# Optimization experiments

Hardware: AMD Instinct MI355X
Metric: run time of the kernel (lower is better)

## Reference

```python
import jax, jax.numpy as jnp
import numpy as np


def setup_inputs() -> dict:
    key = jax.random.key(0)
    kq, kc = jax.random.split(key)
    query = jax.random.normal(kq, (64, 768), dtype=jnp.float32)
    corpus = jax.random.normal(kc, (500000, 768), dtype=jnp.float32)
    return {"query": query, "corpus": corpus, "k": 16}


def reference(query, corpus, k):
    # cosine similarity: (q @ c.T) / (|q|[:,None] * |c|[None,:])  -> [B, N]
    sim = jnp.einsum("bd,nd->bn", query, corpus)
    qn = jnp.linalg.norm(query, axis=1)   # [B]
    cn = jnp.linalg.norm(corpus, axis=1)  # [N]
    sim = sim / (qn[:, None] * cn[None, :])
    # top-k most similar corpus entries per query (largest=True)
    values, indices = jax.lax.top_k(sim, k)  # [B, k], [B, k]
    return values, indices
```

## Files before the change

kernel.cpp:

```cpp
#include <hip/hip_runtime.h>
#include <hip/hip_bf16.h>

#define D 768
#define NQ 64
#define NT 128
#define KC 64
#define NCH (D / KC)
#define TPB 256
#define SIMSTRIDE 133
#define NS 8

typedef float    f32x4 __attribute__((ext_vector_type(4)));
typedef _Float16 h16x8 __attribute__((ext_vector_type(8)));

typedef const void __attribute__((address_space(1)))* gas_ptr;
typedef void __attribute__((address_space(3)))* las_ptr;

__device__ __forceinline__ bool kbetter(float v1, int i1, float v2, int i2) {
    return (v1 > v2) || (v1 == v2 && i1 < i2);
}

__device__ __forceinline__ void topk_insert(float (&tv)[16], int (&ti)[16], float v, int idx) {
    if (!kbetter(v, idx, tv[15], ti[15])) return;
    tv[15] = v; ti[15] = idx;
    #pragma unroll
    for (int s = 15; s >= 1; --s) {
        bool sw = kbetter(tv[s], ti[s], tv[s-1], ti[s-1]);
        float av = sw ? tv[s] : tv[s-1];
        float bv = sw ? tv[s-1] : tv[s];
        int   ai = sw ? ti[s] : ti[s-1];
        int   bi = sw ? ti[s-1] : ti[s];
        tv[s-1] = av; tv[s] = bv; ti[s-1] = ai; ti[s] = bi;
    }
}

__device__ __forceinline__ void bitonic16(float (&v)[16], int (&ix)[16]) {
    #pragma unroll
    for (int d = 8; d >= 1; d >>= 1) {
        #pragma unroll
        for (int i = 0; i < 16; ++i) {
            if ((i & d) == 0) {
                int j = i | d;
                bool sw = kbetter(v[j], ix[j], v[i], ix[i]);
                float av = sw ? v[j] : v[i];
                float bv = sw ? v[i] : v[j];
                int   ai = sw ? ix[j] : ix[i];
                int   bi = sw ? ix[i] : ix[j];
                v[i] = av; v[j] = bv; ix[i] = ai; ix[j] = bi;
            }
        }
    }
}

__device__ __forceinline__ void lane_merge(float (&v)[16], int (&ix)[16], int mask) {
    float pv[16]; int pix[16];
    #pragma unroll
    for (int i = 0; i < 16; ++i) {
        pv[i]  = __shfl_xor(v[15 - i], mask);
        pix[i] = __shfl_xor(ix[15 - i], mask);
    }
    #pragma unroll
    for (int i = 0; i < 16; ++i) {
        if (kbetter(pv[i], pix[i], v[i], ix[i])) { v[i] = pv[i]; ix[i] = pix[i]; }
    }
    bitonic16(v, ix);
}

__device__ __forceinline__ void sort64(float& v, int& ix, int l) {
    #pragma unroll
    for (int k = 2; k <= 64; k <<= 1) {
        #pragma unroll
        for (int j = k >> 1; j >= 1; j >>= 1) {
            float ov = __shfl_xor(v, j);
            int   oi = __shfl_xor(ix, j);
            bool dirDesc = ((l & k) == 0);
            bool lower   = ((l & j) == 0);
            bool takeBetter = (lower == dirDesc);
            bool ob = kbetter(ov, oi, v, ix);
            if (takeBetter == ob) { v = ov; ix = oi; }
        }
    }
}

__global__ __launch_bounds__(256)
void prep_kernel(const float* __restrict__ query, _Float16* __restrict__ qfh,
                 _Float16* __restrict__ qfl) {
    int b = blockIdx.x, t = threadIdx.x;
    const float* row = query + b * D;
    float vals[3]; float s = 0.f;
    #pragma unroll
    for (int j = 0; j < 3; ++j) { vals[j] = row[t + 256 * j]; s += vals[j] * vals[j]; }
    #pragma unroll
    for (int m = 1; m < 64; m <<= 1) s += __shfl_xor(s, m);
    __shared__ float ws4[4];
    if ((t & 63) == 0) ws4[t >> 6] = s;
    __syncthreads();
    float qn = sqrtf(ws4[0] + ws4[1] + ws4[2] + ws4[3]);
    int qf = b >> 4;
    #pragma unroll
    for (int j = 0; j < 3; ++j) {
        int col = t + 256 * j;
        float vn = vals[j] / qn;
        _Float16 h = (_Float16)vn;
        float r = vn - (float)h;
        _Float16 l2 = (_Float16)(r * 2048.0f);
        int cc = col >> 6, kk = (col >> 5) & 1, unit = (col >> 3) & 3, sub = col & 7;
        int lane = (b & 15) + unit * 16;
        size_t off = ((((size_t)cc * 2 + kk) * 4 + qf) * 64 + lane) * 8 + sub;
        qfh[off] = h;
        qfl[off] = l2;
    }
}

__global__ __launch_bounds__(TPB, 2)
void sim_topk_kernel(const float* __restrict__ corpus,
                     const _Float16* __restrict__ qfh,
                     const _Float16* __restrict__ qfl,
                     float2* __restrict__ cand,
                     int N, int NB) {
    __shared__ __align__(16) float lds[2 * NT * KC];
    int t = threadIdx.x, w = t >> 6, l = t & 63;
    int b = blockIdx.x;
    long n0 = (long)b * NT;

    f32x4 accH[4][2], accX[4][2];
    #pragma unroll
    for (int qf = 0; qf < 4; ++qf)
        #pragma unroll
        for (int nfl = 0; nfl < 2; ++nfl) { accH[qf][nfl] = (f32x4)(0.f); accX[qf][nfl] = (f32x4)(0.f); }
    float psum[2] = {0.f, 0.f};

    auto STAGE = [&](int c, int buf) {
        #pragma unroll
        for (int j = 0; j < 8; ++j) {
            int U = t + TPB * j;
            int row = U >> 4, unit = U & 15;
            long grow = n0 + row; if (grow >= N) grow = N - 1;
            int su = unit ^ (row & 15);
            const float* src = corpus + (size_t)grow * D + c * KC + su * 4;
            float* dst = &lds[buf * (NT * KC) + (size_t)U * 4];
            __builtin_amdgcn_global_load_lds((gas_ptr)(const void*)src, (las_ptr)(void*)dst, 16, 0, 0);
        }
    };

    STAGE(0, 0);
    __syncthreads();

    for (int c = 0; c < NCH; ++c) {
        int buf = c & 1;
        if (c + 1 < NCH) STAGE(c + 1, buf ^ 1);

        const float* bufp = &lds[buf * (NT * KC)];
        #pragma unroll
        for (int kk = 0; kk < 2; ++kk) {
            h16x8 qh[4], ql[4];
            #pragma unroll
            for (int qf = 0; qf < 4; ++qf) {
                size_t qoff = ((((size_t)c * 2 + kk) * 4 + qf) * 64 + l) * 8;
                qh[qf] = *(const h16x8*)(qfh + qoff);
                ql[qf] = *(const h16x8*)(qfl + qoff);
            }
            #pragma unroll
            for (int nfl = 0; nfl < 2; ++nfl) {
                int row = w * 32 + nfl * 16 + (l & 15);
                int u0 = kk * 8 + ((l >> 4) << 1);
                f32x4 x0 = *(const f32x4*)(bufp + row * KC + ((u0 ^ (row & 15)) << 2));
                f32x4 x1 = *(const f32x4*)(bufp + row * KC + (((u0 + 1) ^ (row & 15)) << 2));
                h16x8 hi, lo;
                float ps = 0.f;
                #pragma unroll
                for (int i2 = 0; i2 < 4; ++i2) {
                    float v0 = x0[i2]; _Float16 h0 = (_Float16)v0;
                    hi[i2] = h0; lo[i2] = (_Float16)((v0 - (float)h0) * 2048.0f);
                    ps += v0 * v0;
                    float v1 = x1[i2]; _Float16 h1 = (_Float16)v1;
                    hi[4 + i2] = h1; lo[4 + i2] = (_Float16)((v1 - (float)h1) * 2048.0f);
                    ps += v1 * v1;
                }
                psum[nfl] += ps;
                #pragma unroll
                for (int qf = 0; qf < 4; ++qf) {
                    accH[qf][nfl] = __builtin_amdgcn_mfma_f32_16x16x32_f16(qh[qf], hi, accH[qf][nfl], 0, 0, 0);
                    accX[qf][nfl] = __builtin_amdgcn_mfma_f32_16x16x32_f16(qh[qf], lo, accX[qf][nfl], 0, 0, 0);
                    accX[qf][nfl] = __builtin_amdgcn_mfma_f32_16x16x32_f16(ql[qf], hi, accX[qf][nfl], 0, 0, 0);
                }
            }
        }
        __syncthreads();
    }

    float cnv[2];
    #pragma unroll
    for (int nfl = 0; nfl < 2; ++nfl) {
        float s = psum[nfl];
        s += __shfl_xor(s, 16);
        s += __shfl_xor(s, 32);
        cnv[nfl] = sqrtf(s);
    }

    float* sim = (float*)lds;
    #pragma unroll
    for (int nfl = 0; nfl < 2; ++nfl) {
        int n = w * 32 + nfl * 16 + (l & 15);
        #pragma unroll
        for (int qf = 0; qf < 4; ++qf) {
            #pragma unroll
            for (int r = 0; r < 4; ++r) {
                int q = qf * 16 + ((l >> 4) << 2) + r;
                float dot = accH[qf][nfl][r] + accX[qf][nfl][r] * (1.0f / 2048.0f);
                sim[q * SIMSTRIDE + n] = dot / cnv[nfl];
            }
        }
    }
    __syncthreads();

    int q = t >> 2, cc = t & 3;
    float tv[16]; int ti[16];
    #pragma unroll
    for (int s = 0; s < 16; ++s) { tv[s] = -INFINITY; ti[s] = 0x7fffffff; }
    for (int i = 0; i < 32; ++i) {
        int n = cc * 32 + i;
        long g = n0 + n;
        if (g < N) topk_insert(tv, ti, sim[q * SIMSTRIDE + n], (int)g);
    }
    lane_merge(tv, ti, 1);
    lane_merge(tv, ti, 2);
    if ((l & 3) == 0) {
        float2* dst = cand + ((size_t)q * NB + b) * 16;
        #pragma unroll
        for (int s = 0; s < 16; ++s) dst[s] = make_float2(tv[s], __int_as_float(ti[s]));
    }
}

__global__ __launch_bounds__(256)
void merge1_kernel(const float2* __restrict__ cand, float2* __restrict__ cand2, int NB) {
    int q = blockIdx.x >> 3, seg = blockIdx.x & (NS - 1);
    int t = threadIdx.x, w = t >> 6, l = t & 63;
    int total = NB * 16;
    int chunk = (total + NS - 1) / NS;
    int e0 = seg * chunk, e1 = min(total, e0 + chunk);
    const float2* src = cand + (size_t)q * total;
    float tv[16]; int ti[16];
    #pragma unroll
    for (int s = 0; s < 16; ++s) { tv[s] = -INFINITY; ti[s] = 0x7fffffff; }
    for (int e = e0 + t; e < e1; e += 256) {
        float2 ce = src[e];
        topk_insert(tv, ti, ce.x, __float_as_int(ce.y));
    }
    lane_merge(tv, ti, 1);  lane_merge(tv, ti, 2);  lane_merge(tv, ti, 4);
    lane_merge(tv, ti, 8);  lane_merge(tv, ti, 16); lane_merge(tv, ti, 32);
    __shared__ float2 stage[64];
    if (l == 0) {
        #pragma unroll
        for (int s = 0; s < 16; ++s) stage[w * 16 + s] = make_float2(tv[s], __int_as_float(ti[s]));
    }
    __syncthreads();
    if (t < 64) {
        float2 ce = stage[t];
        float v = ce.x; int ix = __float_as_int(ce.y);
        sort64(v, ix, t);
        if (t < 16) cand2[((size_t)q * NS + seg) * 16 + t] = make_float2(v, __int_as_float(ix));
    }
}

__global__ __launch_bounds__(64)
void merge2_kernel(const float2* __restrict__ cand2, float* __restrict__ out) {
    int q = blockIdx.x, l = threadIdx.x;
    const float2* src = cand2 + (size_t)q * (NS * 16);
    float2 a = src[l], b = src[l + 64];
    float v1 = a.x; int i1 = __float_as_int(a.y);
    float v2 = b.x; int i2 = __float_as_int(b.y);
    sort64(v1, i1, l);
    sort64(v2, i2, l);
    float sv = __shfl(v2, (l - 16) & 63);
    int   si = __shfl(i2, (l - 16) & 63);
    float mv = (l < 16) ? v1 : ((l < 32) ? sv : -INFINITY);
    int   mi = (l < 16) ? i1 : ((l < 32) ? si : 0x7fffffff);
    sort64(mv, mi, l);
    if (l < 16) {
        out[q * 16 + l]           = mv;
        out[NQ * 16 + q * 16 + l] = (float)mi;
    }
}

extern "C" void kernel_launch(void* const* d_in, const int* in_sizes, int n_in,
                              void* d_out, int out_size, void* d_ws, size_t ws_size,
                              hipStream_t stream) {
    const float* query  = (const float*)d_in[0];
    const float* corpus = (const float*)d_in[1];
    int N  = in_sizes[1] / D;
    int NB = (N + NT - 1) / NT;
    char* ws = (char*)d_ws;
    _Float16* qfh = (_Float16*)ws;
    _Float16* qfl = (_Float16*)(ws + 98304);
    float2*  cand = (float2*)(ws + 196608);
    size_t candBytes = (size_t)NQ * NB * 16 * sizeof(float2);
    float2* cand2 = (float2*)(ws + 196608 + candBytes);
    float*   out  = (float*)d_out;

    prep_kernel<<<NQ, 256, 0, stream>>>(query, qfh, qfl);
    sim_topk_kernel<<<NB, TPB, 0, stream>>>(corpus, qfh, qfl, cand, N, NB);
    merge1_kernel<<<NQ * NS, 256, 0, stream>>>(cand, cand2, NB);
    merge2_kernel<<<NQ, 64, 0, stream>>>(cand2, out);
}
```

Before: 512.3 us.

## Make similarity kernel persistent with 4-deep LDS pipeline and manual waitcnt scheduling

The sim_topk kernel becomes persistent: a fixed grid of 256 blocks of 512 threads walks contiguous ranges of 64-row corpus tiles. Each tile is split into six 128-wide K chunks, staged through a 4-buffer ring in dynamic LDS with direct global-to-LDS loads. Query fragments are double-buffered in registers, and explicit vmcnt waits plus raw barriers keep loads in flight across tile boundaries. The aim is to hide HBM latency and launch/tail overhead. The cost is twice as many per-tile candidates for the merge stage, plus fragile hand-tuned wait counts.

```diff
diff --git a/kernel.cpp b/kernel.cpp
--- a/kernel.cpp
+++ b/kernel.cpp
@@ -3,12 +3,19 @@
 
 #define D 768
 #define NQ 64
-#define NT 128
-#define KC 64
-#define NCH (D / KC)
-#define TPB 256
-#define SIMSTRIDE 133
+#define NT 64
+#define KC 128
+#define NCHT 6
+#define TPB 512
+#define NBUF 4
+#define SIMST 65
 #define NS 8
+#define GRID 256
+
+#define LDS_BUF_F   (NT * KC)
+#define LDS_SIM_F   (NBUF * LDS_BUF_F)
+#define LDS_CN_F    (LDS_SIM_F + NQ * SIMST)
+#define LDS_BYTES   ((LDS_CN_F + NT) * 4)
 
 typedef float    f32x4 __attribute__((ext_vector_type(4)));
 typedef _Float16 h16x8 __attribute__((ext_vector_type(8)));
@@ -104,139 +111,173 @@
         _Float16 h = (_Float16)vn;
         float r = vn - (float)h;
         _Float16 l2 = (_Float16)(r * 2048.0f);
-        int cc = col >> 6, kk = (col >> 5) & 1, unit = (col >> 3) & 3, sub = col & 7;
+        int cm = col >> 7, ks = (col >> 5) & 3, unit = (col >> 3) & 3, sub = col & 7;
         int lane = (b & 15) + unit * 16;
-        size_t off = ((((size_t)cc * 2 + kk) * 4 + qf) * 64 + lane) * 8 + sub;
+        size_t off = ((((size_t)cm * 4 + ks) * 4 + qf) * 64 + lane) * 8 + sub;
         qfh[off] = h;
         qfl[off] = l2;
     }
 }
+
+struct QF { h16x8 h[2][4]; h16x8 l[2][4]; };
 
 __global__ __launch_bounds__(TPB, 2)
 void sim_topk_kernel(const float* __restrict__ corpus,
                      const _Float16* __restrict__ qfh,
                      const _Float16* __restrict__ qfl,
                      float2* __restrict__ cand,
-                     int N, int NB) {
-    __shared__ __align__(16) float lds[2 * NT * KC];
+                     int N, int NTILES) {
+    extern __shared__ __align__(16) float lds[];
+    float* simF = lds + LDS_SIM_F;
+    float* cnF  = lds + LDS_CN_F;
+
     int t = threadIdx.x, w = t >> 6, l = t & 63;
+    int qfp = w >> 2, nfl = w & 3;
     int b = blockIdx.x;
-    long n0 = (long)b * NT;
-
-    f32x4 accH[4][2], accX[4][2];
-    #pragma unroll
-    for (int qf = 0; qf < 4; ++qf)
-        #pragma unroll
-        for (int nfl = 0; nfl < 2; ++nfl) { accH[qf][nfl] = (f32x4)(0.f); accX[qf][nfl] = (f32x4)(0.f); }
-    float psum[2] = {0.f, 0.f};
-
-    auto STAGE = [&](int c, int buf) {
-        #pragma unroll
-        for (int j = 0; j < 8; ++j) {
-            int U = t + TPB * j;
-            int row = U >> 4, unit = U & 15;
-            long grow = n0 + row; if (grow >= N) grow = N - 1;
-            int su = unit ^ (row & 15);
-            const float* src = corpus + (size_t)grow * D + c * KC + su * 4;
-            float* dst = &lds[buf * (NT * KC) + (size_t)U * 4];
+    int q0 = NTILES / GRID, R = NTILES % GRID;
+    int tstart = b * q0 + min(b, R);
+    int cnt = q0 + (b < R ? 1 : 0);
+    int NC = cnt * NCHT;
+
+    f32x4 accH[2], accX[2];
+    #pragma unroll
+    for (int j = 0; j < 2; ++j) { accH[j] = (f32x4)(0.f); accX[j] = (f32x4)(0.f); }
+    float psum = 0.f;
+
+    QF qA, qB;
+
+    auto QLOAD = [&](int cmq, QF& qd) {
+        #pragma unroll
+        for (int ks = 0; ks < 4; ++ks)
+            #pragma unroll
+            for (int j = 0; j < 2; ++j) {
+                size_t off = ((((size_t)cmq * 4 + ks) * 4 + (qfp * 2 + j)) * 64 + l) * 8;
+                qd.h[j][ks] = *(const h16x8*)(qfh + off);
+                qd.l[j][ks] = *(const h16x8*)(qfl + off);
+            }
+    };
+
+    auto STAGE = [&](int k) {
+        int tile = tstart + k / NCHT;
+        int cm = k % NCHT;
+        float* dbase = lds + (k & 3) * LDS_BUF_F;
+        #pragma unroll
+        for (int jj = 0; jj < 4; ++jj) {
+            int U = t + TPB * jj;
+            int row = U >> 5, g = U & 31;
+            int grow = tile * NT + row;
+            if (grow > N - 1) grow = N - 1;
+            int gs = g ^ (row & 7);
+            const float* src = corpus + (size_t)grow * D + cm * KC + gs * 4;
+            float* dst = dbase + (size_t)U * 4;
             __builtin_amdgcn_global_load_lds((gas_ptr)(const void*)src, (las_ptr)(void*)dst, 16, 0, 0);
         }
     };
 
-    STAGE(0, 0);
-    __syncthreads();
-
-    for (int c = 0; c < NCH; ++c) {
-        int buf = c & 1;
-        if (c + 1 < NCH) STAGE(c + 1, buf ^ 1);
-
-        const float* bufp = &lds[buf * (NT * KC)];
-        #pragma unroll
-        for (int kk = 0; kk < 2; ++kk) {
-            h16x8 qh[4], ql[4];
-            #pragma unroll
-            for (int qf = 0; qf < 4; ++qf) {
-                size_t qoff = ((((size_t)c * 2 + kk) * 4 + qf) * 64 + l) * 8;
-                qh[qf] = *(const h16x8*)(qfh + qoff);
-                ql[qf] = *(const h16x8*)(qfl + qoff);
-            }
-            #pragma unroll
-            for (int nfl = 0; nfl < 2; ++nfl) {
-                int row = w * 32 + nfl * 16 + (l & 15);
-                int u0 = kk * 8 + ((l >> 4) << 1);
-                f32x4 x0 = *(const f32x4*)(bufp + row * KC + ((u0 ^ (row & 15)) << 2));
-                f32x4 x1 = *(const f32x4*)(bufp + row * KC + (((u0 + 1) ^ (row & 15)) << 2));
-                h16x8 hi, lo;
-                float ps = 0.f;
-                #pragma unroll
-                for (int i2 = 0; i2 < 4; ++i2) {
-                    float v0 = x0[i2]; _Float16 h0 = (_Float16)v0;
-                    hi[i2] = h0; lo[i2] = (_Float16)((v0 - (float)h0) * 2048.0f);
-                    ps += v0 * v0;
-                    float v1 = x1[i2]; _Float16 h1 = (_Float16)v1;
-                    hi[4 + i2] = h1; lo[4 + i2] = (_Float16)((v1 - (float)h1) * 2048.0f);
-                    ps += v1 * v1;
-                }
-                psum[nfl] += ps;
-                #pragma unroll
-                for (int qf = 0; qf < 4; ++qf) {
-                    accH[qf][nfl] = __builtin_amdgcn_mfma_f32_16x16x32_f16(qh[qf], hi, accH[qf][nfl], 0, 0, 0);
-                    accX[qf][nfl] = __builtin_amdgcn_mfma_f32_16x16x32_f16(qh[qf], lo, accX[qf][nfl], 0, 0, 0);
-                    accX[qf][nfl] = __builtin_amdgcn_mfma_f32_16x16x32_f16(ql[qf], hi, accX[qf][nfl], 0, 0, 0);
-                }
-            }
-        }
-        __syncthreads();
-    }
-
-    float cnv[2];
-    #pragma unroll
-    for (int nfl = 0; nfl < 2; ++nfl) {
-        float s = psum[nfl];
+    auto COMPUTE = [&](int bidx, QF& qc) {
+        const float* bp = lds + bidx * LDS_BUF_F;
+        int rw = nfl * 16 + (l & 15);
+        int cg = l >> 4;
+        #pragma unroll
+        for (int ks = 0; ks < 4; ++ks) {
+            int g0 = ks * 8 + cg * 2;
+            f32x4 x0 = *(const f32x4*)(bp + rw * KC + ((g0 ^ (rw & 7)) << 2));
+            f32x4 x1 = *(const f32x4*)(bp + rw * KC + (((g0 + 1) ^ (rw & 7)) << 2));
+            h16x8 hi, lo;
+            float ps = 0.f;
+            #pragma unroll
+            for (int i2 = 0; i2 < 4; ++i2) {
+                float v0 = x0[i2]; _Float16 h0 = (_Float16)v0;
+                hi[i2] = h0; lo[i2] = (_Float16)((v0 - (float)h0) * 2048.0f);
+                ps += v0 * v0;
+                float v1 = x1[i2]; _Float16 h1 = (_Float16)v1;
+                hi[4 + i2] = h1; lo[4 + i2] = (_Float16)((v1 - (float)h1) * 2048.0f);
+                ps += v1 * v1;
+            }
+            if (qfp == 0) psum += ps;
+            #pragma unroll
+            for (int j = 0; j < 2; ++j) {
+                accH[j] = __builtin_amdgcn_mfma_f32_16x16x32_f16(qc.h[j][ks], hi, accH[j], 0, 0, 0);
+                accX[j] = __builtin_amdgcn_mfma_f32_16x16x32_f16(qc.h[j][ks], lo, accX[j], 0, 0, 0);
+                accX[j] = __builtin_amdgcn_mfma_f32_16x16x32_f16(qc.l[j][ks], hi, accX[j], 0, 0, 0);
+            }
+        }
+    };
+
+    auto TAIL = [&](int tile) {
+        float s = psum;
         s += __shfl_xor(s, 16);
         s += __shfl_xor(s, 32);
-        cnv[nfl] = sqrtf(s);
-    }
-
-    float* sim = (float*)lds;
-    #pragma unroll
-    for (int nfl = 0; nfl < 2; ++nfl) {
-        int n = w * 32 + nfl * 16 + (l & 15);
-        #pragma unroll
-        for (int qf = 0; qf < 4; ++qf) {
+        if (qfp == 0 && l < 16) cnF[nfl * 16 + l] = sqrtf(s);
+        asm volatile("s_waitcnt lgkmcnt(0)" ::: "memory");
+        __builtin_amdgcn_s_barrier();
+        int n = nfl * 16 + (l & 15);
+        float inv = 1.0f / cnF[n];
+        #pragma unroll
+        for (int j = 0; j < 2; ++j)
             #pragma unroll
             for (int r = 0; r < 4; ++r) {
-                int q = qf * 16 + ((l >> 4) << 2) + r;
-                float dot = accH[qf][nfl][r] + accX[qf][nfl][r] * (1.0f / 2048.0f);
-                sim[q * SIMSTRIDE + n] = dot / cnv[nfl];
-            }
-        }
-    }
-    __syncthreads();
-
-    int q = t >> 2, cc = t & 3;
-    float tv[16]; int ti[16];
-    #pragma unroll
-    for (int s = 0; s < 16; ++s) { tv[s] = -INFINITY; ti[s] = 0x7fffffff; }
-    for (int i = 0; i < 32; ++i) {
-        int n = cc * 32 + i;
-        long g = n0 + n;
-        if (g < N) topk_insert(tv, ti, sim[q * SIMSTRIDE + n], (int)g);
-    }
-    lane_merge(tv, ti, 1);
-    lane_merge(tv, ti, 2);
-    if ((l & 3) == 0) {
-        float2* dst = cand + ((size_t)q * NB + b) * 16;
-        #pragma unroll
-        for (int s = 0; s < 16; ++s) dst[s] = make_float2(tv[s], __int_as_float(ti[s]));
+                int q = qfp * 32 + j * 16 + (l >> 4) * 4 + r;
+                float dot = accH[j][r] + accX[j][r] * (1.0f / 2048.0f);
+                simF[q * SIMST + n] = dot * inv;
+            }
+        asm volatile("s_waitcnt lgkmcnt(0)" ::: "memory");
+        __builtin_amdgcn_s_barrier();
+        int q = t >> 3, sl = t & 7;
+        float tv[16]; int ti[16];
+        #pragma unroll
+        for (int s2 = 0; s2 < 16; ++s2) { tv[s2] = -INFINITY; ti[s2] = 0x7fffffff; }
+        #pragma unroll
+        for (int i = 0; i < 8; ++i) {
+            int n2 = sl * 8 + i;
+            int g = tile * NT + n2;
+            if (g < N) topk_insert(tv, ti, simF[q * SIMST + n2], g);
+        }
+        lane_merge(tv, ti, 1); lane_merge(tv, ti, 2); lane_merge(tv, ti, 4);
+        if (sl == 0) {
+            float2* dst = cand + ((size_t)q * NTILES + tile) * 16;
+            #pragma unroll
+            for (int s2 = 0; s2 < 16; ++s2) dst[s2] = make_float2(tv[s2], __int_as_float(ti[s2]));
+        }
+        #pragma unroll
+        for (int j = 0; j < 2; ++j) { accH[j] = (f32x4)(0.f); accX[j] = (f32x4)(0.f); }
+        psum = 0.f;
+    };
+
+    auto BODY = [&](int cc, QF& qc, QF& qn) {
+        int cm = cc % NCHT;
+        if (cc + 1 < NC) QLOAD((cc + 1) % NCHT, qn);
+        if (cc + 2 < NC) STAGE(cc + 2);
+        if (cc == 0) {
+            asm volatile("s_waitcnt vmcnt(20)" ::: "memory");
+        } else if (cc + 2 >= NC) {
+            if (cc + 1 < NC) { asm volatile("s_waitcnt vmcnt(20)" ::: "memory"); }
+            else             { asm volatile("s_waitcnt vmcnt(0)"  ::: "memory"); }
+        } else if (cm == 0) {
+            asm volatile("s_waitcnt vmcnt(40)" ::: "memory");
+        } else {
+            asm volatile("s_waitcnt vmcnt(24)" ::: "memory");
+        }
+        __builtin_amdgcn_sched_barrier(0);
+        __builtin_amdgcn_s_barrier();
+        __builtin_amdgcn_sched_barrier(0);
+        COMPUTE(cc & 3, qc);
+        if (cm == NCHT - 1) TAIL(tstart + cc / NCHT);
+    };
+
+    STAGE(0); STAGE(1); QLOAD(0, qA);
+    int half = NC >> 1;
+    for (int m = 0; m < half; ++m) {
+        BODY(2 * m,     qA, qB);
+        BODY(2 * m + 1, qB, qA);
     }
 }
 
 __global__ __launch_bounds__(256)
-void merge1_kernel(const float2* __restrict__ cand, float2* __restrict__ cand2, int NB) {
+void merge1_kernel(const float2* __restrict__ cand, float2* __restrict__ cand2, int NTILES) {
     int q = blockIdx.x >> 3, seg = blockIdx.x & (NS - 1);
     int t = threadIdx.x, w = t >> 6, l = t & 63;
-    int total = NB * 16;
+    int total = NTILES * 16;
     int chunk = (total + NS - 1) / NS;
     int e0 = seg * chunk, e1 = min(total, e0 + chunk);
     const float2* src = cand + (size_t)q * total;
@@ -288,18 +329,21 @@
                               hipStream_t stream) {
     const float* query  = (const float*)d_in[0];
     const float* corpus = (const float*)d_in[1];
-    int N  = in_sizes[1] / D;
-    int NB = (N + NT - 1) / NT;
+    int N      = in_sizes[1] / D;
+    int NTILES = (N + NT - 1) / NT;
     char* ws = (char*)d_ws;
     _Float16* qfh = (_Float16*)ws;
     _Float16* qfl = (_Float16*)(ws + 98304);
     float2*  cand = (float2*)(ws + 196608);
-    size_t candBytes = (size_t)NQ * NB * 16 * sizeof(float2);
+    size_t candBytes = (size_t)NQ * NTILES * 16 * sizeof(float2);
     float2* cand2 = (float2*)(ws + 196608 + candBytes);
     float*   out  = (float*)d_out;
 
+    (void)hipFuncSetAttribute((const void*)sim_topk_kernel,
+                              hipFuncAttributeMaxDynamicSharedMemorySize, LDS_BYTES);
+
     prep_kernel<<<NQ, 256, 0, stream>>>(query, qfh, qfl);
-    sim_topk_kernel<<<NB, TPB, 0, stream>>>(corpus, qfh, qfl, cand, N, NB);
-    merge1_kernel<<<NQ * NS, 256, 0, stream>>>(cand, cand2, NB);
+    sim_topk_kernel<<<GRID, TPB, LDS_BYTES, stream>>>(corpus, qfh, qfl, cand, N, NTILES);
+    merge1_kernel<<<NQ * NS, 256, 0, stream>>>(cand, cand2, NTILES);
     merge2_kernel<<<NQ, 64, 0, stream>>>(cand2, out);
 }
```

Result: slower. 752.6 us (+46.9%).

## Convert corpus to fp16 hi/lo once at staging and use 512-thread blocks

Applied to the files above, without the earlier changes.

Corpus tiles are no longer copied straight into LDS as fp32 with global_load_lds. Each chunk is now loaded into registers, split into fp16 hi/lo halves once, and written to padded LDS buffers, while the next chunk's global loads overlap the MFMA work on the current one. Block size doubles to 512 threads with one 16-row fragment per wave, corpus norms go through LDS, and top-k uses 8 lanes per query. The aim is to stop each wave redoing the fp32-to-fp16 split and to raise occupancy, at the cost of more VGPR pressure from register staging and an extra LDS round trip.

```diff
diff --git a/kernel.cpp b/kernel.cpp
--- a/kernel.cpp
+++ b/kernel.cpp
@@ -5,16 +5,20 @@
 #define NQ 64
 #define NT 128
 #define KC 64
-#define NCH (D / KC)
-#define TPB 256
-#define SIMSTRIDE 133
+#define NCHT 12
+#define TPB 512
+#define SIMST 133
 #define NS 8
+
+#define HST 72
+#define BUF_HALVES (NT * HST)
+#define BUF_STRIDE (2 * BUF_HALVES)
+#define LDS_CN_BYTE (2 * BUF_STRIDE * 2)
+#define LDS_BYTES (LDS_CN_BYTE + NT * 4)
 
 typedef float    f32x4 __attribute__((ext_vector_type(4)));
 typedef _Float16 h16x8 __attribute__((ext_vector_type(8)));
-
-typedef const void __attribute__((address_space(1)))* gas_ptr;
-typedef void __attribute__((address_space(3)))* las_ptr;
+typedef _Float16 h16x4 __attribute__((ext_vector_type(4)));
 
 __device__ __forceinline__ bool kbetter(float v1, int i1, float v2, int i2) {
     return (v1 > v2) || (v1 == v2 && i1 < i2);
@@ -112,131 +116,138 @@
     }
 }
 
-__global__ __launch_bounds__(TPB, 2)
+__global__ __launch_bounds__(TPB, 4)
 void sim_topk_kernel(const float* __restrict__ corpus,
                      const _Float16* __restrict__ qfh,
                      const _Float16* __restrict__ qfl,
                      float2* __restrict__ cand,
-                     int N, int NB) {
-    __shared__ __align__(16) float lds[2 * NT * KC];
+                     int N, int NTILES) {
+    extern __shared__ __align__(16) char smem[];
+    _Float16* bufs = (_Float16*)smem;
+    float*    cnF  = (float*)(smem + LDS_CN_BYTE);
+    float*    simF = (float*)smem;
+
     int t = threadIdx.x, w = t >> 6, l = t & 63;
     int b = blockIdx.x;
     long n0 = (long)b * NT;
 
-    f32x4 accH[4][2], accX[4][2];
-    #pragma unroll
-    for (int qf = 0; qf < 4; ++qf)
-        #pragma unroll
-        for (int nfl = 0; nfl < 2; ++nfl) { accH[qf][nfl] = (f32x4)(0.f); accX[qf][nfl] = (f32x4)(0.f); }
-    float psum[2] = {0.f, 0.f};
-
-    auto STAGE = [&](int c, int buf) {
-        #pragma unroll
-        for (int j = 0; j < 8; ++j) {
-            int U = t + TPB * j;
-            int row = U >> 4, unit = U & 15;
-            long grow = n0 + row; if (grow >= N) grow = N - 1;
-            int su = unit ^ (row & 15);
-            const float* src = corpus + (size_t)grow * D + c * KC + su * 4;
-            float* dst = &lds[buf * (NT * KC) + (size_t)U * 4];
-            __builtin_amdgcn_global_load_lds((gas_ptr)(const void*)src, (las_ptr)(void*)dst, 16, 0, 0);
+    f32x4 accH[4], accX[4];
+    #pragma unroll
+    for (int qf = 0; qf < 4; ++qf) { accH[qf] = (f32x4)(0.f); accX[qf] = (f32x4)(0.f); }
+    float psum[4] = {0.f, 0.f, 0.f, 0.f};
+
+    int rw = w * 16 + (l & 15);
+    int cg = l >> 4;
+
+    auto LOADSTG = [&](int c, float4 (&stg)[4]) {
+        #pragma unroll
+        for (int jj = 0; jj < 4; ++jj) {
+            int U = t + TPB * jj;
+            int r = U >> 4, u = U & 15;
+            long grow = n0 + r; if (grow > N - 1) grow = N - 1;
+            stg[jj] = *(const float4*)(corpus + (size_t)grow * D + c * KC + u * 4);
         }
     };
 
-    STAGE(0, 0);
-    __syncthreads();
-
-    for (int c = 0; c < NCH; ++c) {
-        int buf = c & 1;
-        if (c + 1 < NCH) STAGE(c + 1, buf ^ 1);
-
-        const float* bufp = &lds[buf * (NT * KC)];
-        #pragma unroll
-        for (int kk = 0; kk < 2; ++kk) {
-            h16x8 qh[4], ql[4];
+    auto CONV = [&](float4 (&stg)[4], int buf) {
+        _Float16* bh = bufs + buf * BUF_STRIDE;
+        _Float16* blo = bh + BUF_HALVES;
+        #pragma unroll
+        for (int jj = 0; jj < 4; ++jj) {
+            int U = t + TPB * jj;
+            int r = U >> 4, u = U & 15;
+            float4 x = stg[jj];
+            psum[jj] += x.x * x.x + x.y * x.y + x.z * x.z + x.w * x.w;
+            h16x4 h, lo;
+            h.x = (_Float16)x.x; h.y = (_Float16)x.y; h.z = (_Float16)x.z; h.w = (_Float16)x.w;
+            lo.x = (_Float16)((x.x - (float)h.x) * 2048.0f);
+            lo.y = (_Float16)((x.y - (float)h.y) * 2048.0f);
+            lo.z = (_Float16)((x.z - (float)h.z) * 2048.0f);
+            lo.w = (_Float16)((x.w - (float)h.w) * 2048.0f);
+            *(h16x4*)(bh  + r * HST + u * 4) = h;
+            *(h16x4*)(blo + r * HST + u * 4) = lo;
+        }
+    };
+
+    {
+        float4 stg[4];
+        LOADSTG(0, stg);
+        CONV(stg, 0);
+    }
+    __syncthreads();
+
+    for (int c = 0; c < NCHT; ++c) {
+        h16x8 qh[2][4], ql[2][4];
+        #pragma unroll
+        for (int kk = 0; kk < 2; ++kk)
             #pragma unroll
             for (int qf = 0; qf < 4; ++qf) {
                 size_t qoff = ((((size_t)c * 2 + kk) * 4 + qf) * 64 + l) * 8;
-                qh[qf] = *(const h16x8*)(qfh + qoff);
-                ql[qf] = *(const h16x8*)(qfl + qoff);
+                qh[kk][qf] = *(const h16x8*)(qfh + qoff);
+                ql[kk][qf] = *(const h16x8*)(qfl + qoff);
             }
+        float4 stg[4];
+        if (c + 1 < NCHT) LOADSTG(c + 1, stg);
+        const _Float16* bh = bufs + (c & 1) * BUF_STRIDE;
+        const _Float16* blo = bh + BUF_HALVES;
+        #pragma unroll
+        for (int kk = 0; kk < 2; ++kk) {
+            h16x8 ch = *(const h16x8*)(bh  + rw * HST + kk * 32 + cg * 8);
+            h16x8 cl = *(const h16x8*)(blo + rw * HST + kk * 32 + cg * 8);
             #pragma unroll
-            for (int nfl = 0; nfl < 2; ++nfl) {
-                int row = w * 32 + nfl * 16 + (l & 15);
-                int u0 = kk * 8 + ((l >> 4) << 1);
-                f32x4 x0 = *(const f32x4*)(bufp + row * KC + ((u0 ^ (row & 15)) << 2));
-                f32x4 x1 = *(const f32x4*)(bufp + row * KC + (((u0 + 1) ^ (row & 15)) << 2));
-                h16x8 hi, lo;
-                float ps = 0.f;
-                #pragma unroll
-                for (int i2 = 0; i2 < 4; ++i2) {
-                    float v0 = x0[i2]; _Float16 h0 = (_Float16)v0;
-                    hi[i2] = h0; lo[i2] = (_Float16)((v0 - (float)h0) * 2048.0f);
-                    ps += v0 * v0;
-                    float v1 = x1[i2]; _Float16 h1 = (_Float16)v1;
-                    hi[4 + i2] = h1; lo[4 + i2] = (_Float16)((v1 - (float)h1) * 2048.0f);
-                    ps += v1 * v1;
-                }
-                psum[nfl] += ps;
-                #pragma unroll
-                for (int qf = 0; qf < 4; ++qf) {
-                    accH[qf][nfl] = __builtin_amdgcn_mfma_f32_16x16x32_f16(qh[qf], hi, accH[qf][nfl], 0, 0, 0);
-                    accX[qf][nfl] = __builtin_amdgcn_mfma_f32_16x16x32_f16(qh[qf], lo, accX[qf][nfl], 0, 0, 0);
-                    accX[qf][nfl] = __builtin_amdgcn_mfma_f32_16x16x32_f16(ql[qf], hi, accX[qf][nfl], 0, 0, 0);
-                }
+            for (int qf = 0; qf < 4; ++qf) {
+                accH[qf] = __builtin_amdgcn_mfma_f32_16x16x32_f16(qh[kk][qf], ch, accH[qf], 0, 0, 0);
+                accX[qf] = __builtin_amdgcn_mfma_f32_16x16x32_f16(qh[kk][qf], cl, accX[qf], 0, 0, 0);
+                accX[qf] = __builtin_amdgcn_mfma_f32_16x16x32_f16(ql[kk][qf], ch, accX[qf], 0, 0, 0);
             }
         }
+        if (c + 1 < NCHT) CONV(stg, (c + 1) & 1);
         __syncthreads();
     }
 
-    float cnv[2];
-    #pragma unroll
-    for (int nfl = 0; nfl < 2; ++nfl) {
-        float s = psum[nfl];
-        s += __shfl_xor(s, 16);
-        s += __shfl_xor(s, 32);
-        cnv[nfl] = sqrtf(s);
-    }
-
-    float* sim = (float*)lds;
-    #pragma unroll
-    for (int nfl = 0; nfl < 2; ++nfl) {
-        int n = w * 32 + nfl * 16 + (l & 15);
-        #pragma unroll
-        for (int qf = 0; qf < 4; ++qf) {
-            #pragma unroll
-            for (int r = 0; r < 4; ++r) {
-                int q = qf * 16 + ((l >> 4) << 2) + r;
-                float dot = accH[qf][nfl][r] + accX[qf][nfl][r] * (1.0f / 2048.0f);
-                sim[q * SIMSTRIDE + n] = dot / cnv[nfl];
-            }
-        }
-    }
-    __syncthreads();
-
-    int q = t >> 2, cc = t & 3;
+    #pragma unroll
+    for (int jj = 0; jj < 4; ++jj) {
+        float s = psum[jj];
+        s += __shfl_xor(s, 1); s += __shfl_xor(s, 2);
+        s += __shfl_xor(s, 4); s += __shfl_xor(s, 8);
+        if ((t & 15) == 0) cnF[(t >> 4) + 32 * jj] = sqrtf(s);
+    }
+    __syncthreads();
+    float inv = 1.0f / cnF[rw];
+    __syncthreads();
+    #pragma unroll
+    for (int qf = 0; qf < 4; ++qf)
+        #pragma unroll
+        for (int r = 0; r < 4; ++r) {
+            int q = qf * 16 + cg * 4 + r;
+            float dot = accH[qf][r] + accX[qf][r] * (1.0f / 2048.0f);
+            simF[q * SIMST + rw] = dot * inv;
+        }
+    __syncthreads();
+
+    int q = t >> 3, sl = t & 7;
     float tv[16]; int ti[16];
     #pragma unroll
-    for (int s = 0; s < 16; ++s) { tv[s] = -INFINITY; ti[s] = 0x7fffffff; }
-    for (int i = 0; i < 32; ++i) {
-        int n = cc * 32 + i;
+    for (int s2 = 0; s2 < 16; ++s2) { tv[s2] = -INFINITY; ti[s2] = 0x7fffffff; }
+    #pragma unroll
+    for (int i = 0; i < 16; ++i) {
+        int n = sl * 16 + i;
         long g = n0 + n;
-        if (g < N) topk_insert(tv, ti, sim[q * SIMSTRIDE + n], (int)g);
-    }
-    lane_merge(tv, ti, 1);
-    lane_merge(tv, ti, 2);
-    if ((l & 3) == 0) {
-        float2* dst = cand + ((size_t)q * NB + b) * 16;
-        #pragma unroll
-        for (int s = 0; s < 16; ++s) dst[s] = make_float2(tv[s], __int_as_float(ti[s]));
+        if (g < N) topk_insert(tv, ti, simF[q * SIMST + n], (int)g);
+    }
+    lane_merge(tv, ti, 1); lane_merge(tv, ti, 2); lane_merge(tv, ti, 4);
+    if (sl == 0) {
+        float2* dst = cand + ((size_t)q * NTILES + b) * 16;
+        #pragma unroll
+        for (int s2 = 0; s2 < 16; ++s2) dst[s2] = make_float2(tv[s2], __int_as_float(ti[s2]));
     }
 }
 
 __global__ __launch_bounds__(256)
-void merge1_kernel(const float2* __restrict__ cand, float2* __restrict__ cand2, int NB) {
+void merge1_kernel(const float2* __restrict__ cand, float2* __restrict__ cand2, int NTILES) {
     int q = blockIdx.x >> 3, seg = blockIdx.x & (NS - 1);
     int t = threadIdx.x, w = t >> 6, l = t & 63;
-    int total = NB * 16;
+    int total = NTILES * 16;
     int chunk = (total + NS - 1) / NS;
     int e0 = seg * chunk, e1 = min(total, e0 + chunk);
     const float2* src = cand + (size_t)q * total;
@@ -288,18 +299,21 @@
                               hipStream_t stream) {
     const float* query  = (const float*)d_in[0];
     const float* corpus = (const float*)d_in[1];
-    int N  = in_sizes[1] / D;
-    int NB = (N + NT - 1) / NT;
+    int N      = in_sizes[1] / D;
+    int NTILES = (N + NT - 1) / NT;
     char* ws = (char*)d_ws;
     _Float16* qfh = (_Float16*)ws;
     _Float16* qfl = (_Float16*)(ws + 98304);
     float2*  cand = (float2*)(ws + 196608);
-    size_t candBytes = (size_t)NQ * NB * 16 * sizeof(float2);
+    size_t candBytes = (size_t)NQ * NTILES * 16 * sizeof(float2);
     float2* cand2 = (float2*)(ws + 196608 + candBytes);
     float*   out  = (float*)d_out;
 
+    (void)hipFuncSetAttribute((const void*)sim_topk_kernel,
+                              hipFuncAttributeMaxDynamicSharedMemorySize, LDS_BYTES);
+
     prep_kernel<<<NQ, 256, 0, stream>>>(query, qfh, qfl);
-    sim_topk_kernel<<<NB, TPB, 0, stream>>>(corpus, qfh, qfl, cand, N, NB);
-    merge1_kernel<<<NQ * NS, 256, 0, stream>>>(cand, cand2, NB);
+    sim_topk_kernel<<<NTILES, TPB, LDS_BYTES, stream>>>(corpus, qfh, qfl, cand, N, NTILES);
+    merge1_kernel<<<NQ * NS, 256, 0, stream>>>(cand, cand2, NTILES);
     merge2_kernel<<<NQ, 64, 0, stream>>>(cand2, out);
 }
```

Measured after the change: 641.1 us. +25.1%, slower.

## Restructure similarity kernel into persistent per-wave tiles with register top-k

Applied to the files above, without the earlier changes.

Replaces the block-tiled kernel, which staged 128 corpus rows in LDS, with a persistent grid where each wave handles 32-row groups. Each wave loads corpus data directly from global memory into registers, runs the split-fp16 MFMAs, and keeps a running per-query top-16 in registers across groups. Each wave writes out one candidate list at the end instead of one per block, and the hi/lo query fragments are packed together. The aim is to remove LDS staging and block barriers and to shrink the candidate traffic. The cost is uncoalesced direct global loads, no explicit prefetch pipeline, and serial top-k insertion on every tile.

```diff
diff --git a/kernel.cpp b/kernel.cpp
--- a/kernel.cpp
+++ b/kernel.cpp
@@ -3,18 +3,15 @@
 
 #define D 768
 #define NQ 64
-#define NT 128
-#define KC 64
-#define NCH (D / KC)
 #define TPB 256
-#define SIMSTRIDE 133
+#define GRID 1303
+#define NWAVES (GRID * 4)
+#define KSTEPS 24
+#define SIMP 20
 #define NS 8
 
 typedef float    f32x4 __attribute__((ext_vector_type(4)));
 typedef _Float16 h16x8 __attribute__((ext_vector_type(8)));
-
-typedef const void __attribute__((address_space(1)))* gas_ptr;
-typedef void __attribute__((address_space(3)))* las_ptr;
 
 __device__ __forceinline__ bool kbetter(float v1, int i1, float v2, int i2) {
     return (v1 > v2) || (v1 == v2 && i1 < i2);
@@ -83,8 +80,7 @@
 }
 
 __global__ __launch_bounds__(256)
-void prep_kernel(const float* __restrict__ query, _Float16* __restrict__ qfh,
-                 _Float16* __restrict__ qfl) {
+void prep_kernel(const float* __restrict__ query, _Float16* __restrict__ qpk) {
     int b = blockIdx.x, t = threadIdx.x;
     const float* row = query + b * D;
     float vals[3]; float s = 0.f;
@@ -104,139 +100,140 @@
         _Float16 h = (_Float16)vn;
         float r = vn - (float)h;
         _Float16 l2 = (_Float16)(r * 2048.0f);
-        int cc = col >> 6, kk = (col >> 5) & 1, unit = (col >> 3) & 3, sub = col & 7;
+        int ks = col >> 5, unit = (col >> 3) & 3, sub = col & 7;
         int lane = (b & 15) + unit * 16;
-        size_t off = ((((size_t)cc * 2 + kk) * 4 + qf) * 64 + lane) * 8 + sub;
-        qfh[off] = h;
-        qfl[off] = l2;
+        size_t off = (((size_t)ks * 4 + qf) * 64 + lane) * 16 + sub;
+        qpk[off]     = h;
+        qpk[off + 8] = l2;
     }
 }
 
 __global__ __launch_bounds__(TPB, 2)
 void sim_topk_kernel(const float* __restrict__ corpus,
-                     const _Float16* __restrict__ qfh,
-                     const _Float16* __restrict__ qfl,
+                     const _Float16* __restrict__ qpk,
                      float2* __restrict__ cand,
-                     int N, int NB) {
-    __shared__ __align__(16) float lds[2 * NT * KC];
+                     int N, int NG) {
+    __shared__ float scratch[4][NQ * SIMP];
     int t = threadIdx.x, w = t >> 6, l = t & 63;
-    int b = blockIdx.x;
-    long n0 = (long)b * NT;
-
-    f32x4 accH[4][2], accX[4][2];
-    #pragma unroll
-    for (int qf = 0; qf < 4; ++qf)
-        #pragma unroll
-        for (int nfl = 0; nfl < 2; ++nfl) { accH[qf][nfl] = (f32x4)(0.f); accX[qf][nfl] = (f32x4)(0.f); }
-    float psum[2] = {0.f, 0.f};
-
-    auto STAGE = [&](int c, int buf) {
-        #pragma unroll
-        for (int j = 0; j < 8; ++j) {
-            int U = t + TPB * j;
-            int row = U >> 4, unit = U & 15;
-            long grow = n0 + row; if (grow >= N) grow = N - 1;
-            int su = unit ^ (row & 15);
-            const float* src = corpus + (size_t)grow * D + c * KC + su * 4;
-            float* dst = &lds[buf * (NT * KC) + (size_t)U * 4];
-            __builtin_amdgcn_global_load_lds((gas_ptr)(const void*)src, (las_ptr)(void*)dst, 16, 0, 0);
-        }
-    };
-
-    STAGE(0, 0);
-    __syncthreads();
-
-    for (int c = 0; c < NCH; ++c) {
-        int buf = c & 1;
-        if (c + 1 < NCH) STAGE(c + 1, buf ^ 1);
-
-        const float* bufp = &lds[buf * (NT * KC)];
-        #pragma unroll
-        for (int kk = 0; kk < 2; ++kk) {
+    int ww = blockIdx.x * 4 + w;
+    int n16 = l & 15, kg = l >> 4;
+    float* sc = scratch[w];
+
+    float tv[16]; int ti[16];
+    #pragma unroll
+    for (int s = 0; s < 16; ++s) { tv[s] = -INFINITY; ti[s] = 0x7fffffff; }
+
+    for (int g = ww; g < NG; g += NWAVES) {
+        long baseA = (long)g * 32;
+        long rA = baseA + n16;      if (rA > N - 1) rA = N - 1;
+        long rB = baseA + 16 + n16; if (rB > N - 1) rB = N - 1;
+        const float* pA = corpus + (size_t)rA * D + kg * 8;
+        const float* pB = corpus + (size_t)rB * D + kg * 8;
+
+        f32x4 accAH[4], accAX[4], accBH[4], accBX[4];
+        #pragma unroll
+        for (int qf = 0; qf < 4; ++qf) {
+            accAH[qf] = (f32x4)(0.f); accAX[qf] = (f32x4)(0.f);
+            accBH[qf] = (f32x4)(0.f); accBX[qf] = (f32x4)(0.f);
+        }
+        float psA = 0.f, psB = 0.f;
+
+        #pragma unroll 2
+        for (int ks = 0; ks < KSTEPS; ++ks) {
             h16x8 qh[4], ql[4];
             #pragma unroll
             for (int qf = 0; qf < 4; ++qf) {
-                size_t qoff = ((((size_t)c * 2 + kk) * 4 + qf) * 64 + l) * 8;
-                qh[qf] = *(const h16x8*)(qfh + qoff);
-                ql[qf] = *(const h16x8*)(qfl + qoff);
-            }
-            #pragma unroll
-            for (int nfl = 0; nfl < 2; ++nfl) {
-                int row = w * 32 + nfl * 16 + (l & 15);
-                int u0 = kk * 8 + ((l >> 4) << 1);
-                f32x4 x0 = *(const f32x4*)(bufp + row * KC + ((u0 ^ (row & 15)) << 2));
-                f32x4 x1 = *(const f32x4*)(bufp + row * KC + (((u0 + 1) ^ (row & 15)) << 2));
-                h16x8 hi, lo;
-                float ps = 0.f;
+                const _Float16* qp = qpk + (((size_t)ks * 4 + qf) * 64 + l) * 16;
+                qh[qf] = *(const h16x8*)qp;
+                ql[qf] = *(const h16x8*)(qp + 8);
+            }
+            f32x4 a0 = *(const f32x4*)(pA + ks * 32);
+            f32x4 a1 = *(const f32x4*)(pA + ks * 32 + 4);
+            f32x4 b0 = *(const f32x4*)(pB + ks * 32);
+            f32x4 b1 = *(const f32x4*)(pB + ks * 32 + 4);
+
+            h16x8 hiA, loA, hiB, loB;
+            #pragma unroll
+            for (int i = 0; i < 4; ++i) {
+                float va = a0[i]; _Float16 ha = (_Float16)va;
+                hiA[i] = ha; loA[i] = (_Float16)((va - (float)ha) * 2048.0f);
+                psA += va * va;
+                float va1 = a1[i]; _Float16 ha1 = (_Float16)va1;
+                hiA[4 + i] = ha1; loA[4 + i] = (_Float16)((va1 - (float)ha1) * 2048.0f);
+                psA += va1 * va1;
+                float vb = b0[i]; _Float16 hb = (_Float16)vb;
+                hiB[i] = hb; loB[i] = (_Float16)((vb - (float)hb) * 2048.0f);
+                psB += vb * vb;
+                float vb1 = b1[i]; _Float16 hb1 = (_Float16)vb1;
+                hiB[4 + i] = hb1; loB[4 + i] = (_Float16)((vb1 - (float)hb1) * 2048.0f);
+                psB += vb1 * vb1;
+            }
+            #pragma unroll
+            for (int qf = 0; qf < 4; ++qf) {
+                accAH[qf] = __builtin_amdgcn_mfma_f32_16x16x32_f16(qh[qf], hiA, accAH[qf], 0, 0, 0);
+                accAX[qf] = __builtin_amdgcn_mfma_f32_16x16x32_f16(qh[qf], loA, accAX[qf], 0, 0, 0);
+                accAX[qf] = __builtin_amdgcn_mfma_f32_16x16x32_f16(ql[qf], hiA, accAX[qf], 0, 0, 0);
+                accBH[qf] = __builtin_amdgcn_mfma_f32_16x16x32_f16(qh[qf], hiB, accBH[qf], 0, 0, 0);
+                accBX[qf] = __builtin_amdgcn_mfma_f32_16x16x32_f16(qh[qf], loB, accBX[qf], 0, 0, 0);
+                accBX[qf] = __builtin_amdgcn_mfma_f32_16x16x32_f16(ql[qf], hiB, accBX[qf], 0, 0, 0);
+            }
+        }
+
+        psA += __shfl_xor(psA, 16); psA += __shfl_xor(psA, 32);
+        psB += __shfl_xor(psB, 16); psB += __shfl_xor(psB, 32);
+        float invA = 1.0f / sqrtf(psA);
+        float invB = 1.0f / sqrtf(psB);
+
+        #pragma unroll
+        for (int qf = 0; qf < 4; ++qf)
+            #pragma unroll
+            for (int r = 0; r < 4; ++r) {
+                int q = qf * 16 + kg * 4 + r;
+                sc[q * SIMP + n16] = (accAH[qf][r] + accAX[qf][r] * (1.0f / 2048.0f)) * invA;
+            }
+        {
+            f32x4 sv[4];
+            #pragma unroll
+            for (int j = 0; j < 4; ++j) sv[j] = *(const f32x4*)(sc + l * SIMP + j * 4);
+            #pragma unroll
+            for (int j = 0; j < 4; ++j)
                 #pragma unroll
-                for (int i2 = 0; i2 < 4; ++i2) {
-                    float v0 = x0[i2]; _Float16 h0 = (_Float16)v0;
-                    hi[i2] = h0; lo[i2] = (_Float16)((v0 - (float)h0) * 2048.0f);
-                    ps += v0 * v0;
-                    float v1 = x1[i2]; _Float16 h1 = (_Float16)v1;
-                    hi[4 + i2] = h1; lo[4 + i2] = (_Float16)((v1 - (float)h1) * 2048.0f);
-                    ps += v1 * v1;
+                for (int e = 0; e < 4; ++e) {
+                    long gidx = baseA + j * 4 + e;
+                    if (gidx < N) topk_insert(tv, ti, sv[j][e], (int)gidx);
                 }
-                psum[nfl] += ps;
+        }
+        #pragma unroll
+        for (int qf = 0; qf < 4; ++qf)
+            #pragma unroll
+            for (int r = 0; r < 4; ++r) {
+                int q = qf * 16 + kg * 4 + r;
+                sc[q * SIMP + n16] = (accBH[qf][r] + accBX[qf][r] * (1.0f / 2048.0f)) * invB;
+            }
+        {
+            f32x4 sv[4];
+            #pragma unroll
+            for (int j = 0; j < 4; ++j) sv[j] = *(const f32x4*)(sc + l * SIMP + j * 4);
+            #pragma unroll
+            for (int j = 0; j < 4; ++j)
                 #pragma unroll
-                for (int qf = 0; qf < 4; ++qf) {
-                    accH[qf][nfl] = __builtin_amdgcn_mfma_f32_16x16x32_f16(qh[qf], hi, accH[qf][nfl], 0, 0, 0);
-                    accX[qf][nfl] = __builtin_amdgcn_mfma_f32_16x16x32_f16(qh[qf], lo, accX[qf][nfl], 0, 0, 0);
-                    accX[qf][nfl] = __builtin_amdgcn_mfma_f32_16x16x32_f16(ql[qf], hi, accX[qf][nfl], 0, 0, 0);
+                for (int e = 0; e < 4; ++e) {
+                    long gidx = baseA + 16 + j * 4 + e;
+                    if (gidx < N) topk_insert(tv, ti, sv[j][e], (int)gidx);
                 }
-            }
-        }
-        __syncthreads();
-    }
-
-    float cnv[2];
-    #pragma unroll
-    for (int nfl = 0; nfl < 2; ++nfl) {
-        float s = psum[nfl];
-        s += __shfl_xor(s, 16);
-        s += __shfl_xor(s, 32);
-        cnv[nfl] = sqrtf(s);
-    }
-
-    float* sim = (float*)lds;
-    #pragma unroll
-    for (int nfl = 0; nfl < 2; ++nfl) {
-        int n = w * 32 + nfl * 16 + (l & 15);
-        #pragma unroll
-        for (int qf = 0; qf < 4; ++qf) {
-            #pragma unroll
-            for (int r = 0; r < 4; ++r) {
-                int q = qf * 16 + ((l >> 4) << 2) + r;
-                float dot = accH[qf][nfl][r] + accX[qf][nfl][r] * (1.0f / 2048.0f);
-                sim[q * SIMSTRIDE + n] = dot / cnv[nfl];
-            }
-        }
-    }
-    __syncthreads();
-
-    int q = t >> 2, cc = t & 3;
-    float tv[16]; int ti[16];
-    #pragma unroll
-    for (int s = 0; s < 16; ++s) { tv[s] = -INFINITY; ti[s] = 0x7fffffff; }
-    for (int i = 0; i < 32; ++i) {
-        int n = cc * 32 + i;
-        long g = n0 + n;
-        if (g < N) topk_insert(tv, ti, sim[q * SIMSTRIDE + n], (int)g);
-    }
-    lane_merge(tv, ti, 1);
-    lane_merge(tv, ti, 2);
-    if ((l & 3) == 0) {
-        float2* dst = cand + ((size_t)q * NB + b) * 16;
-        #pragma unroll
-        for (int s = 0; s < 16; ++s) dst[s] = make_float2(tv[s], __int_as_float(ti[s]));
-    }
+        }
+    }
+
+    float2* dst = cand + ((size_t)l * NWAVES + ww) * 16;
+    #pragma unroll
+    for (int s = 0; s < 16; ++s) dst[s] = make_float2(tv[s], __int_as_float(ti[s]));
 }
 
 __global__ __launch_bounds__(256)
-void merge1_kernel(const float2* __restrict__ cand, float2* __restrict__ cand2, int NB) {
+void merge1_kernel(const float2* __restrict__ cand, float2* __restrict__ cand2, int NWV) {
     int q = blockIdx.x >> 3, seg = blockIdx.x & (NS - 1);
     int t = threadIdx.x, w = t >> 6, l = t & 63;
-    int total = NB * 16;
+    int total = NWV * 16;
     int chunk = (total + NS - 1) / NS;
     int e0 = seg * chunk, e1 = min(total, e0 + chunk);
     const float2* src = cand + (size_t)q * total;
@@ -289,17 +286,16 @@
     const float* query  = (const float*)d_in[0];
     const float* corpus = (const float*)d_in[1];
     int N  = in_sizes[1] / D;
-    int NB = (N + NT - 1) / NT;
+    int NG = (N + 31) / 32;
     char* ws = (char*)d_ws;
-    _Float16* qfh = (_Float16*)ws;
-    _Float16* qfl = (_Float16*)(ws + 98304);
+    _Float16* qpk = (_Float16*)ws;
     float2*  cand = (float2*)(ws + 196608);
-    size_t candBytes = (size_t)NQ * NB * 16 * sizeof(float2);
+    size_t candBytes = (size_t)NQ * NWAVES * 16 * sizeof(float2);
     float2* cand2 = (float2*)(ws + 196608 + candBytes);
     float*   out  = (float*)d_out;
 
-    prep_kernel<<<NQ, 256, 0, stream>>>(query, qfh, qfl);
-    sim_topk_kernel<<<NB, TPB, 0, stream>>>(corpus, qfh, qfl, cand, N, NB);
-    merge1_kernel<<<NQ * NS, 256, 0, stream>>>(cand, cand2, NB);
+    prep_kernel<<<NQ, 256, 0, stream>>>(query, qpk);
+    sim_topk_kernel<<<GRID, TPB, 0, stream>>>(corpus, qpk, cand, N, NG);
+    merge1_kernel<<<NQ * NS, 256, 0, stream>>>(cand, cand2, NWAVES);
     merge2_kernel<<<NQ, 64, 0, stream>>>(cand2, out);
 }
```

Result: slower. 614.2 us (+19.9%).
